# Kernel optimization log

Hardware: AMD Instinct MI355X
Metric: run time of the kernel (lower is better)

Reference implementation:

```python
import jax, jax.numpy as jnp
import numpy as np

NX = 768
N_HEAD = 12
N_CTX = 2048
MASKED_BIAS = -10000.0


def setup_inputs() -> dict:
    key = jax.random.key(0)
    ks = jax.random.split(key, 6)
    bs, seq = 2, N_CTX
    hidden_states = jax.random.normal(ks[0], (bs, seq, NX), dtype=jnp.float32)
    attention_mask = jnp.zeros((bs, 1, 1, seq), dtype=jnp.float32)
    # Conv1D params: out = x @ W + b, W: (in, out)
    w_attn = jax.random.normal(ks[1], (NX, 3 * NX), dtype=jnp.float32) * 0.02
    b_attn = jnp.zeros((3 * NX,), dtype=jnp.float32)
    w_proj = jax.random.normal(ks[2], (NX, NX), dtype=jnp.float32) * 0.02
    b_proj = jnp.zeros((NX,), dtype=jnp.float32)
    return {
        "hidden_states": hidden_states,
        "attention_mask": attention_mask,
        "w_attn": w_attn,
        "b_attn": b_attn,
        "w_proj": w_proj,
        "b_proj": b_proj,
    }


def reference(hidden_states, attention_mask, w_attn, b_attn, w_proj, b_proj):
    bs, seq, _ = hidden_states.shape
    hd = NX // N_HEAD  # 64
    qkv = hidden_states @ w_attn + b_attn  # [bs, seq, 3*nx]
    query, key, value = jnp.split(qkv, 3, axis=2)
    # Faithful to source: direct reshape (NOT standard split-heads transpose)
    q = query.reshape(bs, N_HEAD, seq, hd)
    k = key.reshape(bs, N_HEAD, seq, hd)
    v = value.reshape(bs, N_HEAD, seq, hd)
    w = jnp.einsum("bhqd,bhkd->bhqk", q, k) / jnp.sqrt(jnp.float32(hd))
    # causal mask: tril, sliced as bias[:, :, ns-nd:ns, :ns] with nd=ns=seq
    mask = jnp.tril(jnp.ones((seq, seq), dtype=jnp.float32))[None, None]
    w = w * mask + MASKED_BIAS * (1.0 - mask)
    w = w + attention_mask
    w = jax.nn.softmax(w, axis=-1)  # dropout = identity (eval mode)
    a = jnp.einsum("bhqk,bhkd->bhqd", w, v)
    a = a.transpose(0, 2, 1, 3).reshape(bs, seq, NX)
    a = a @ w_proj + b_proj  # resid dropout = identity
    return a
```

## Files before the change

kernel.cpp:

```cpp
#include <hip/hip_runtime.h>
#include <hip/hip_bf16.h>

typedef unsigned short u16;
typedef short bf16x8 __attribute__((ext_vector_type(8)));
typedef float f32x4 __attribute__((ext_vector_type(4)));

#define NXC 768
#define NHEAD 12
#define SEQ 2048
#define BSZ 2
#define HD 64
#define NCHUNK 72
#define LOG2E 1.4426950408889634f

__device__ inline u16 f2bf(float f) {
    unsigned int u = __float_as_uint(f);
    unsigned int r = u + 0x7fffu + ((u >> 16) & 1u);
    return (u16)(r >> 16);
}
__device__ inline unsigned pk2(float lo, float hi) {
    return (unsigned)f2bf(lo) | ((unsigned)f2bf(hi) << 16);
}
__device__ inline float ex2(float x) { return __builtin_amdgcn_exp2f(x); }

__device__ inline void gld16(const u16* g, u16* l) {
    __builtin_amdgcn_global_load_lds(
        (const __attribute__((address_space(1))) unsigned int*)(g),
        (__attribute__((address_space(3))) unsigned int*)(l),
        16, 0, 0);
}

__global__ void cast4_kernel(const float* __restrict__ in, u16* __restrict__ out, int n4) {
    int i = blockIdx.x * 256 + threadIdx.x;
    if (i >= n4) return;
    float4 v = ((const float4*)in)[i];
    ushort4 o;
    o.x = f2bf(v.x); o.y = f2bf(v.y); o.z = f2bf(v.z); o.w = f2bf(v.w);
    ((ushort4*)out)[i] = o;
}

__global__ void transpose_cast_kernel(const float* __restrict__ in, u16* __restrict__ out,
                                      int R, int C) {
    __shared__ float tile[32][33];
    int cb = blockIdx.x * 32, rb = blockIdx.y * 32;
    int tx = threadIdx.x, ty = threadIdx.y;
    #pragma unroll
    for (int i = 0; i < 32; i += 8)
        tile[ty + i][tx] = in[(size_t)(rb + ty + i) * C + cb + tx];
    __syncthreads();
    #pragma unroll
    for (int i = 0; i < 32; i += 8)
        out[(size_t)(cb + ty + i) * R + rb + tx] = f2bf(tile[tx][ty + i]);
}

__global__ __launch_bounds__(256) void vt_kernel(const u16* __restrict__ Vb,
                                                 u16* __restrict__ Vtg) {
    __shared__ u16 tile[64][68];
    int y = blockIdx.y;
    size_t base = (size_t)y * (SEQ * HD);
    int ss0 = blockIdx.x * 64;
    int t = threadIdx.x;
    #pragma unroll
    for (int c = t; c < 512; c += 256) {
        int r = c >> 3, col = (c & 7) * 8;
        *(uint4*)&tile[r][col] = *(const uint4*)&Vb[base + (size_t)(ss0 + r) * HD + col];
    }
    __syncthreads();
    #pragma unroll
    for (int c = t; c < 512; c += 256) {
        int dd = c >> 3, s8 = (c & 7) * 8;
        ushort4 a, bq;
        a.x = tile[s8 + 0][dd]; a.y = tile[s8 + 1][dd];
        a.z = tile[s8 + 2][dd]; a.w = tile[s8 + 3][dd];
        bq.x = tile[s8 + 4][dd]; bq.y = tile[s8 + 5][dd];
        bq.z = tile[s8 + 6][dd]; bq.w = tile[s8 + 7][dd];
        u16* dst = &Vtg[base + (size_t)dd * SEQ + ss0 + s8];
        *(ushort4*)dst = a;
        *(ushort4*)(dst + 4) = bq;
    }
}

template <int EPI>
__global__ __launch_bounds__(256) void gemm_bt_kernel(
    const u16* __restrict__ A, const u16* __restrict__ BT,
    const float* __restrict__ bias,
    u16* __restrict__ outQ, u16* __restrict__ outK, u16* __restrict__ outV,
    float* __restrict__ outF,
    int M, int N, int K) {
    __shared__ u16 As[128 * 32];
    __shared__ u16 Bs[128 * 32];
    int tileM = blockIdx.y * 128, tileN = blockIdx.x * 128;
    int t = threadIdx.x;
    int lane = t & 63, wave = t >> 6;
    int wr = (wave >> 1) * 64, wc = (wave & 1) * 64;
    int quad = lane >> 4, l16 = lane & 15;
    f32x4 acc[4][4] = {};

    int r0 = t >> 2, c0 = (t & 3) * 8;
    const u16* Ag0 = A + (size_t)(tileM + r0) * K + c0;
    const u16* Ag1 = Ag0 + (size_t)64 * K;
    const u16* Bg0 = BT + (size_t)(tileN + r0) * K + c0;
    const u16* Bg1 = Bg0 + (size_t)64 * K;
    u16* AsW0 = As + wave * 512;
    u16* AsW1 = As + 2048 + wave * 512;
    u16* BsW0 = Bs + wave * 512;
    u16* BsW1 = Bs + 2048 + wave * 512;

    for (int k0 = 0; k0 < K; k0 += 32) {
        __syncthreads();
        gld16(Ag0 + k0, AsW0);
        gld16(Ag1 + k0, AsW1);
        gld16(Bg0 + k0, BsW0);
        gld16(Bg1 + k0, BsW1);
        __syncthreads();

        bf16x8 af[4], bfr[4];
        #pragma unroll
        for (int i = 0; i < 4; ++i)
            af[i] = *(const bf16x8*)&As[(wr + i * 16 + l16) * 32 + quad * 8];
        #pragma unroll
        for (int j = 0; j < 4; ++j)
            bfr[j] = *(const bf16x8*)&Bs[(wc + j * 16 + l16) * 32 + quad * 8];
        #pragma unroll
        for (int i = 0; i < 4; ++i)
            #pragma unroll
            for (int j = 0; j < 4; ++j)
                acc[i][j] = __builtin_amdgcn_mfma_f32_16x16x32_bf16(af[i], bfr[j], acc[i][j], 0, 0, 0);
    }

    #pragma unroll
    for (int i = 0; i < 4; ++i) {
        #pragma unroll
        for (int j = 0; j < 4; ++j) {
            int n = tileN + wc + j * 16 + l16;
            float bv = bias[n];
            #pragma unroll
            for (int r = 0; r < 4; ++r) {
                int m = tileM + wr + i * 16 + quad * 4 + r;
                float v = acc[i][j][r] + bv;
                if (EPI == 0) {
                    if (n < 768) {
                        outQ[(size_t)m * 768 + n] = f2bf(v);
                    } else if (n < 1536) {
                        outK[(size_t)m * 768 + (n - 768)] = f2bf(v * (0.125f * LOG2E));
                    } else {
                        outV[(size_t)m * 768 + (n - 1536)] = f2bf(v);
                    }
                } else {
                    outF[(size_t)m * N + n] = v;
                }
            }
        }
    }
}

__global__ __launch_bounds__(512) void attn_mfma_kernel(
    const u16* __restrict__ Q, const u16* __restrict__ Kg,
    const u16* __restrict__ Vtg, const float* __restrict__ amask,
    u16* __restrict__ Opart, float* __restrict__ Lpart) {
    __shared__ u16 Ks[64][72];
    __shared__ u16 Vt[64][72];
    __shared__ u16 Ps[8][16][72];
    __shared__ float Ams[64];

    int bh = blockIdx.y;
    int b = bh / NHEAD, h = bh % NHEAD;
    int p = NCHUNK - 1 - (int)blockIdx.x;
    int bx = 15, c = 0, a = 0;
    #pragma unroll
    for (int i = 0; i < 16; ++i) {
        int n = (i + 2) >> 1;
        if (p < a + n) { bx = i; c = p - a; break; }
        a += n;
    }
    int kbase = c * 256;
    int nt = 2 * (bx + 1) - 4 * c;
    if (nt > 4) nt = 4;

    int t = threadIdx.x;
    int w = t >> 6, lane = t & 63;
    int quad = lane >> 4, l16 = lane & 15;
    size_t headbase = (size_t)b * (SEQ * NXC) + (size_t)h * (SEQ * HD);
    size_t headbaseT = (size_t)(b * NHEAD + h) * (SEQ * HD);

    int r0 = bx * 128;
    int qw0 = r0 + w * 16;
    int qrow = qw0 + l16;
    bf16x8 qf[2];
    #pragma unroll
    for (int s = 0; s < 2; ++s)
        qf[s] = *(const bf16x8*)&Q[headbase + (size_t)(qw0 + l16) * HD + s * 32 + quad * 8];

    float l_part = 0.f;
    f32x4 o[4] = {};

    int pr_row = t >> 3, pr_col = (t & 7) * 8;
    uint4 kr, vr; float amr;
    {
        int k0 = kbase;
        kr = *(const uint4*)&Kg[headbase + (size_t)(k0 + pr_row) * HD + pr_col];
        vr = *(const uint4*)&Vtg[headbaseT + (size_t)pr_row * SEQ + k0 + pr_col];
        if (t < 64) amr = amask[(size_t)b * SEQ + k0 + t];
    }

    for (int kt = 0; kt < nt; ++kt) {
        int k0 = kbase + kt * 64;
        __syncthreads();
        *(uint4*)&Ks[pr_row][pr_col] = kr;
        *(uint4*)&Vt[pr_row][pr_col] = vr;
        if (t < 64) Ams[t] = amr * LOG2E;
        __syncthreads();
        if (kt + 1 < nt) {
            int kn = k0 + 64;
            kr = *(const uint4*)&Kg[headbase + (size_t)(kn + pr_row) * HD + pr_col];
            vr = *(const uint4*)&Vtg[headbaseT + (size_t)pr_row * SEQ + kn + pr_col];
            if (t < 64) amr = amask[(size_t)b * SEQ + kn + t];
        }

        if (k0 > qw0 + 15) continue;

        bf16x8 kf[2][4];
        #pragma unroll
        for (int s = 0; s < 2; ++s)
            #pragma unroll
            for (int j = 0; j < 4; ++j)
                kf[s][j] = *(const bf16x8*)&Ks[j * 16 + l16][s * 32 + quad * 8];
        float amv[4][4];
        #pragma unroll
        for (int j = 0; j < 4; ++j)
            #pragma unroll
            for (int r = 0; r < 4; ++r)
                amv[j][r] = Ams[j * 16 + quad * 4 + r];

        f32x4 sacc[4] = {};
        #pragma unroll
        for (int s = 0; s < 2; ++s)
            #pragma unroll
            for (int j = 0; j < 4; ++j)
                sacc[j] = __builtin_amdgcn_mfma_f32_16x16x32_bf16(kf[s][j], qf[s], sacc[j], 0, 0, 0);

        bool diag = (k0 + 63 > qw0);
        #pragma unroll
        for (int j = 0; j < 4; ++j) {
            float pv[4];
            #pragma unroll
            for (int r = 0; r < 4; ++r) {
                float pp = ex2(sacc[j][r] + amv[j][r]);
                if (diag && (k0 + j * 16 + quad * 4 + r > qrow)) pp = 0.f;
                pv[r] = pp;
            }
            l_part += (pv[0] + pv[1]) + (pv[2] + pv[3]);
            unsigned pk01 = ((__float_as_uint(pv[0]) + 0x8000u) >> 16) |
                            ((__float_as_uint(pv[1]) + 0x8000u) & 0xffff0000u);
            unsigned pk23 = ((__float_as_uint(pv[2]) + 0x8000u) >> 16) |
                            ((__float_as_uint(pv[3]) + 0x8000u) & 0xffff0000u);
            *(uint2*)&Ps[w][l16][j * 16 + quad * 4] = make_uint2(pk01, pk23);
        }

        #pragma unroll
        for (int s = 0; s < 2; ++s) {
            bf16x8 pf = *(const bf16x8*)&Ps[w][l16][s * 32 + quad * 8];
            #pragma unroll
            for (int dc = 0; dc < 4; ++dc) {
                bf16x8 vf = *(const bf16x8*)&Vt[dc * 16 + l16][s * 32 + quad * 8];
                o[dc] = __builtin_amdgcn_mfma_f32_16x16x32_bf16(pf, vf, o[dc], 0, 0, 0);
            }
        }
    }

    float l = l_part + __shfl_xor(l_part, 16);
    l += __shfl_xor(l, 32);
    u16* Ob = Opart + ((size_t)bh * NCHUNK + p) * (128 * 64);
    float* Lb = Lpart + ((size_t)bh * NCHUNK + p) * 128;
    #pragma unroll
    for (int dc = 0; dc < 4; ++dc)
        #pragma unroll
        for (int r = 0; r < 4; ++r) {
            int rl = w * 16 + quad * 4 + r;
            Ob[rl * 64 + dc * 16 + l16] = f2bf(o[dc][r]);
        }
    if (quad == 0) Lb[w * 16 + l16] = l;
}

__global__ __launch_bounds__(256) void attn_combine_kernel(
    const u16* __restrict__ Opart, const float* __restrict__ Lpart,
    u16* __restrict__ Aout) {
    __shared__ float winv[32];
    int bh = blockIdx.y;
    int b = bh / NHEAD, h = bh % NHEAD;
    int row0 = blockIdx.x * 32;
    int bx = row0 >> 7;
    int nch = (bx + 2) >> 1;
    int m = bx >> 1;
    int p0 = (bx & 1) ? (m + 1) * (m + 1) : m * (m + 1);
    int rbase = row0 & 127;
    int t = threadIdx.x;

    if (t < 32) {
        float L = 0.f;
        for (int c = 0; c < nch; ++c)
            L += Lpart[((size_t)bh * NCHUNK + p0 + c) * 128 + rbase + t];
        winv[t] = 1.0f / L;
    }
    __syncthreads();

    int row = t >> 3;
    int d0 = (t & 7) * 8;
    int rl = rbase + row;
    float acc[8] = {};
    for (int c = 0; c < nch; ++c) {
        uint4 u = *(const uint4*)&Opart[(((size_t)bh * NCHUNK + p0 + c) * 128 + rl) * 64 + d0];
        acc[0] += __uint_as_float(u.x << 16);
        acc[1] += __uint_as_float(u.x & 0xffff0000u);
        acc[2] += __uint_as_float(u.y << 16);
        acc[3] += __uint_as_float(u.y & 0xffff0000u);
        acc[4] += __uint_as_float(u.z << 16);
        acc[5] += __uint_as_float(u.z & 0xffff0000u);
        acc[6] += __uint_as_float(u.w << 16);
        acc[7] += __uint_as_float(u.w & 0xffff0000u);
    }
    float s = winv[row];
    uint4 o;
    o.x = pk2(acc[0] * s, acc[1] * s);
    o.y = pk2(acc[2] * s, acc[3] * s);
    o.z = pk2(acc[4] * s, acc[5] * s);
    o.w = pk2(acc[6] * s, acc[7] * s);
    *(uint4*)&Aout[((size_t)b * SEQ + row0 + row) * NXC + h * HD + d0] = o;
}

extern "C" void kernel_launch(void* const* d_in, const int* in_sizes, int n_in,
                              void* d_out, int out_size, void* d_ws, size_t ws_size,
                              hipStream_t stream) {
    const float* hs     = (const float*)d_in[0];
    const float* amask  = (const float*)d_in[1];
    const float* w_attn = (const float*)d_in[2];
    const float* b_attn = (const float*)d_in[3];
    const float* w_proj = (const float*)d_in[4];
    const float* b_proj = (const float*)d_in[5];
    float* out = (float*)d_out;

    const int M = BSZ * SEQ;
    char* ws = (char*)d_ws;
    auto alloc = [&](size_t bytes) {
        char* p = ws;
        ws += (bytes + 255) & ~(size_t)255;
        return p;
    };
    u16* HSbf   = (u16*)alloc((size_t)M * NXC * 2);
    u16* WaT    = (u16*)alloc((size_t)3 * NXC * NXC * 2);
    u16* WpT    = (u16*)alloc((size_t)NXC * NXC * 2);
    u16* Qb     = (u16*)alloc((size_t)M * NXC * 2);
    u16* Kb     = (u16*)alloc((size_t)M * NXC * 2);
    u16* Vb     = (u16*)alloc((size_t)M * NXC * 2);
    u16* Vtg    = (u16*)alloc((size_t)M * NXC * 2);
    u16* Ab     = (u16*)alloc((size_t)M * NXC * 2);
    u16* Opart  = (u16*)alloc((size_t)BSZ * NHEAD * NCHUNK * 128 * 64 * 2);
    float* Lpart = (float*)alloc((size_t)BSZ * NHEAD * NCHUNK * 128 * 4);

    {
        int n4 = M * NXC / 4;
        cast4_kernel<<<dim3((n4 + 255) / 256), dim3(256), 0, stream>>>(hs, HSbf, n4);
        transpose_cast_kernel<<<dim3(3 * NXC / 32, NXC / 32), dim3(32, 8), 0, stream>>>(w_attn, WaT, NXC, 3 * NXC);
        transpose_cast_kernel<<<dim3(NXC / 32, NXC / 32), dim3(32, 8), 0, stream>>>(w_proj, WpT, NXC, NXC);
    }
    gemm_bt_kernel<0><<<dim3(3 * NXC / 128, M / 128), dim3(256), 0, stream>>>(
        HSbf, WaT, b_attn, Qb, Kb, Vb, nullptr, M, 3 * NXC, NXC);
    vt_kernel<<<dim3(SEQ / 64, BSZ * NHEAD), dim3(256), 0, stream>>>(Vb, Vtg);
    attn_mfma_kernel<<<dim3(NCHUNK, BSZ * NHEAD), dim3(512), 0, stream>>>(
        Qb, Kb, Vtg, amask, Opart, Lpart);
    attn_combine_kernel<<<dim3(SEQ / 32, BSZ * NHEAD), dim3(256), 0, stream>>>(
        Opart, Lpart, Ab);
    gemm_bt_kernel<1><<<dim3(NXC / 128, M / 128), dim3(256), 0, stream>>>(
        Ab, WpT, b_proj, nullptr, nullptr, nullptr, out, M, NXC, NXC);
}
```

Measured before the change: 181.8 us.

## Double-buffer LDS tiles in GEMM to overlap global loads with MFMA

Doubles the shared-memory A/B tiles and prefetches the next K-slice through direct global-to-LDS loads while the current slice is consumed by MFMAs. Explicit vmcnt waits and raw s_barriers with sched_barriers replace the pair of __syncthreads per iteration. This is meant to hide global-load latency in the QKV and projection GEMMs. The cost is twice the LDS per block, which may lower occupancy, and correctness now depends on the hand-written waitcnt ordering.

```diff
diff --git a/kernel.cpp b/kernel.cpp
--- a/kernel.cpp
+++ b/kernel.cpp
@@ -87,8 +87,8 @@
     u16* __restrict__ outQ, u16* __restrict__ outK, u16* __restrict__ outV,
     float* __restrict__ outF,
     int M, int N, int K) {
-    __shared__ u16 As[128 * 32];
-    __shared__ u16 Bs[128 * 32];
+    __shared__ u16 As[2 * 128 * 32];
+    __shared__ u16 Bs[2 * 128 * 32];
     int tileM = blockIdx.y * 128, tileN = blockIdx.x * 128;
     int t = threadIdx.x;
     int lane = t & 63, wave = t >> 6;
@@ -106,26 +106,45 @@
     u16* BsW0 = Bs + wave * 512;
     u16* BsW1 = Bs + 2048 + wave * 512;
 
-    for (int k0 = 0; k0 < K; k0 += 32) {
-        __syncthreads();
-        gld16(Ag0 + k0, AsW0);
-        gld16(Ag1 + k0, AsW1);
-        gld16(Bg0 + k0, BsW0);
-        gld16(Bg1 + k0, BsW1);
-        __syncthreads();
-
+    gld16(Ag0, AsW0);
+    gld16(Ag1, AsW1);
+    gld16(Bg0, BsW0);
+    gld16(Bg1, BsW1);
+
+    int NT = K >> 5;
+    for (int tt = 0; tt < NT; ++tt) {
+        int cur = tt & 1;
+        if (tt + 1 < NT) {
+            int kn = (tt + 1) * 32;
+            int nb = (cur ^ 1) * 4096;
+            gld16(Ag0 + kn, AsW0 + nb);
+            gld16(Ag1 + kn, AsW1 + nb);
+            gld16(Bg0 + kn, BsW0 + nb);
+            gld16(Bg1 + kn, BsW1 + nb);
+            asm volatile("s_waitcnt vmcnt(4)" ::: "memory");
+        } else {
+            asm volatile("s_waitcnt vmcnt(0)" ::: "memory");
+        }
+        __builtin_amdgcn_s_barrier();
+        __builtin_amdgcn_sched_barrier(0);
+
+        const u16* Ac = As + cur * 4096;
+        const u16* Bc = Bs + cur * 4096;
         bf16x8 af[4], bfr[4];
         #pragma unroll
         for (int i = 0; i < 4; ++i)
-            af[i] = *(const bf16x8*)&As[(wr + i * 16 + l16) * 32 + quad * 8];
+            af[i] = *(const bf16x8*)&Ac[(wr + i * 16 + l16) * 32 + quad * 8];
         #pragma unroll
         for (int j = 0; j < 4; ++j)
-            bfr[j] = *(const bf16x8*)&Bs[(wc + j * 16 + l16) * 32 + quad * 8];
+            bfr[j] = *(const bf16x8*)&Bc[(wc + j * 16 + l16) * 32 + quad * 8];
         #pragma unroll
         for (int i = 0; i < 4; ++i)
             #pragma unroll
             for (int j = 0; j < 4; ++j)
                 acc[i][j] = __builtin_amdgcn_mfma_f32_16x16x32_bf16(af[i], bfr[j], acc[i][j], 0, 0, 0);
+
+        __builtin_amdgcn_sched_barrier(0);
+        __builtin_amdgcn_s_barrier();
     }
 
     #pragma unroll
```

New measurement: 176.3 us. -3.0%, faster.
